# Kernel optimization log

Hardware: AMD Instinct MI355X
Metric: run time of the kernel (lower is better)

Reference implementation:

```python
import jax, jax.numpy as jnp
import numpy as np

N = 50000      # nodes
E = 800000     # edges (avg degree 16)
G = 256        # graphs in batch
DIN = 126      # input feature dim (hardcoded in module)
H = 128        # dim_h


def _lin_init(key, fan_in, shape):
    s = 1.0 / np.sqrt(fan_in)
    return jax.random.uniform(key, shape, minval=-s, maxval=s, dtype=jnp.float32)


def setup_inputs() -> dict:
    key = jax.random.key(0)
    ks = iter(jax.random.split(key, 64))
    inp = {}
    inp["x"] = jax.random.normal(next(ks), (N, DIN), dtype=jnp.float32)
    inp["edge_attr"] = jax.random.normal(next(ks), (E, 4), dtype=jnp.float32)  # unused by the conv (edge_dim=None)
    dims = [(DIN, H), (H, H), (H, H)]
    for l, (i, o) in enumerate(dims, start=1):
        for nm, bnm in [("Wk", "bk"), ("Wq", "bq"), ("Wv", "bv"), ("Ws", "bs")]:
            inp[f"{nm}{l}"] = _lin_init(next(ks), i, (i, o))
            inp[f"{bnm}{l}"] = _lin_init(next(ks), i, (o,))
    inp["W4"] = _lin_init(next(ks), H, (H, 64))
    inp["b4"] = _lin_init(next(ks), H, (64,))
    inp["W5"] = _lin_init(next(ks), 64, (64, 1))
    inp["b5"] = _lin_init(next(ks), 64, (1,))
    inp["edge_index"] = jax.random.randint(next(ks), (2, E), 0, N, dtype=jnp.int64)
    inp["batch"] = jnp.sort(jax.random.randint(next(ks), (N,), 0, G, dtype=jnp.int64))
    return inp


def _res_gated_conv(x, src, dst, Wk, bk, Wq, bq, Wv, bv, Ws, bs):
    # PyG ResGatedGraphConv: out_i = skip(x_i) + sum_j sigmoid(K_i + Q_j) * V_j
    K = x @ Wk + bk   # [N, H] keys (destination / x_i)
    Q = x @ Wq + bq   # [N, H] queries (source / x_j)
    V = x @ Wv + bv   # [N, H] values (source / x_j)
    gate = jax.nn.sigmoid(K[dst] + Q[src])           # [E, H]
    msg = gate * V[src]                              # [E, H]
    agg = jax.ops.segment_sum(msg, dst, num_segments=x.shape[0])  # scatter-add to dst
    return agg + x @ Ws + bs  # lin_skip (no bias) + conv bias


def reference(x, edge_attr,
              Wk1, bk1, Wq1, bq1, Wv1, bv1, Ws1, bs1,
              Wk2, bk2, Wq2, bq2, Wv2, bv2, Ws2, bs2,
              Wk3, bk3, Wq3, bq3, Wv3, bv3, Ws3, bs3,
              W4, b4, W5, b5, edge_index, batch):
    src, dst = edge_index[0], edge_index[1]
    h = jax.nn.relu(_res_gated_conv(x, src, dst, Wk1, bk1, Wq1, bq1, Wv1, bv1, Ws1, bs1))
    h = jax.nn.relu(_res_gated_conv(h, src, dst, Wk2, bk2, Wq2, bq2, Wv2, bv2, Ws2, bs2))
    h = _res_gated_conv(h, src, dst, Wk3, bk3, Wq3, bq3, Wv3, bv3, Ws3, bs3)
    # global_add_pool over graphs
    hg = jax.ops.segment_sum(h, batch, num_segments=G)  # [G, H]
    hg = jax.nn.relu(hg @ W4 + b4)
    return jax.nn.sigmoid(hg @ W5 + b5)  # [G, 1]
```

## Files before the change

### kernel.cpp

```cpp
#include <hip/hip_runtime.h>

#define N_NODES 50000
#define N_EDGES 800000
#define N_GRAPHS 256
#define DIN 126
#define H 128
#define MP 50048
#define NBKT 196
#define NBA 100
#define CHA 8000

typedef __attribute__((ext_vector_type(8))) _Float16 half8v;
typedef __attribute__((ext_vector_type(4))) _Float16 half4v;
typedef __attribute__((ext_vector_type(4))) float f32x4;
typedef __attribute__((ext_vector_type(2))) float f32x2;

__global__ __launch_bounds__(256) void conv_A(const float* __restrict__ X, int M, int Kd,
                                              _Float16* __restrict__ A16)
{
    const int t = blockIdx.x * 256 + threadIdx.x;
    const int row = t >> 4;
    if (row >= MP) return;
    const int k0 = (t & 15) * 8;
    half8v v8;
    #pragma unroll
    for (int j = 0; j < 8; ++j) {
        const int k = k0 + j;
        float v = 0.f;
        if (row < M && k < Kd) v = X[(size_t)row * Kd + k];
        v8[j] = (_Float16)v;
    }
    *(half8v*)&A16[(size_t)row * 128 + k0] = v8;
}

struct WPtrs { const float* w[12]; };

__global__ __launch_bounds__(256) void conv_W3(WPtrs P, _Float16* __restrict__ Wt16)
{
    const int t = blockIdx.x * 256 + threadIdx.x;
    if (t >= 3 * 512 * 128) return;
    const int layer = t >> 16;
    const int r = t & 65535;
    const int n = r >> 7, k = r & 127;
    const int mtx = n >> 7, cc = n & 127;
    const int Kd = (layer == 0) ? DIN : H;
    const float* W = P.w[layer * 4 + mtx];
    const float v = (k < Kd) ? W[(size_t)k * 128 + cc] : 0.f;
    Wt16[t] = (_Float16)v;
}

__device__ __forceinline__ void dense_out(const uint2 (&ldsO)[64][32],
                                          unsigned char* __restrict__ dst,
                                          int row0, int M, int t)
{
    #pragma unroll
    for (int i = 0; i < 4; ++i) {
        const int idx = i * 256 + t;
        const int rr = idx >> 4, c16 = idx & 15;
        const int ch = c16 ^ ((rr & 15) >> 1);
        const uint2 a = ldsO[rr][2 * ch];
        const uint2 b = ldsO[rr][2 * ch + 1];
        if (row0 + rr < M) {
            uint4 o;
            if (rr & 1) { o.x = b.x; o.y = b.y; o.z = a.x; o.w = a.y; }
            else        { o.x = a.x; o.y = a.y; o.z = b.x; o.w = b.y; }
            *(uint4*)(dst + (size_t)(row0 + rr) * 256 + c16 * 16) = o;
        }
    }
}

__device__ __forceinline__ void compute_acc(const _Float16 (&ldsA)[2][64 * 64],
                                            const _Float16* __restrict__ Wt16,
                                            int mtx, int fr, int kq, int wc,
                                            f32x4 (&acc)[4][2])
{
    #pragma unroll
    for (int step = 0; step < 4; ++step) {
        const int kg = step * 4 + kq;
        const int kh = kg >> 3, kk = kg & 7;
        half8v a[4];
        #pragma unroll
        for (int m = 0; m < 4; ++m) {
            const int ar = m * 16 + fr;
            const int slot = kk ^ (ar & 7);
            a[m] = *(const half8v*)&ldsA[kh][ar * 64 + slot * 8];
        }
        half8v w[2];
        #pragma unroll
        for (int n = 0; n < 2; ++n) {
            const size_t wo = (size_t)(mtx * 128 + wc * 32 + n * 16 + fr) * 128 + kg * 8;
            w[n] = *(const half8v*)&Wt16[wo];
        }
        #pragma unroll
        for (int m = 0; m < 4; ++m)
            #pragma unroll
            for (int n = 0; n < 2; ++n)
                acc[m][n] = __builtin_amdgcn_mfma_f32_16x16x32_f16(w[n], a[m], acc[m][n], 0, 0, 0);
    }
}

__global__ __launch_bounds__(256, 5) void gemm_mfma(
    const _Float16* __restrict__ A16, const _Float16* __restrict__ Wt16,
    const float* __restrict__ bias0, const float* __restrict__ bias1,
    const float* __restrict__ bias2, const float* __restrict__ bias3,
    _Float16* __restrict__ OEK, unsigned char* __restrict__ QV8,
    _Float16* __restrict__ OS, int M)
{
    __shared__ _Float16 ldsA[2][64 * 64];
    __shared__ uint2 ldsO[64][32];
    const int t = threadIdx.x;
    const int l = t & 63, wc = t >> 6;
    const int row0 = blockIdx.x * 64;
    const int mp = blockIdx.y;
    const int fr = l & 15;
    const int kq = l >> 4;

    #pragma unroll
    for (int i = 0; i < 4; ++i) {
        const int gi = i * 256 + t;
        const int kh = gi >> 9;
        const int r = (gi >> 3) & 63;
        const int j = gi & 7;
        const int slot = j ^ (r & 7);
        *(half8v*)&ldsA[kh][r * 64 + slot * 8] =
            *(const half8v*)&A16[(size_t)(row0 + r) * 128 + kh * 64 + j * 8];
    }
    __syncthreads();

    if (mp == 0) {
        {
            f32x4 acc[4][2] = {};
            compute_acc(ldsA, Wt16, 0, fr, kq, wc, acc);
            #pragma unroll
            for (int n = 0; n < 2; ++n) {
                const int c0 = wc * 32 + n * 16 + kq * 4;
                const float4 bv = *(const float4*)&bias0[c0];
                #pragma unroll
                for (int m = 0; m < 4; ++m) {
                    const int rl = m * 16 + fr;
                    half4v o;
                    o[0] = (_Float16)__expf(-(acc[m][n][0] + bv.x));
                    o[1] = (_Float16)__expf(-(acc[m][n][1] + bv.y));
                    o[2] = (_Float16)__expf(-(acc[m][n][2] + bv.z));
                    o[3] = (_Float16)__expf(-(acc[m][n][3] + bv.w));
                    ldsO[rl][(c0 >> 2) ^ fr] = *(uint2*)&o;
                }
            }
        }
        __syncthreads();
        dense_out(ldsO, (unsigned char*)OEK, row0, M, t);
        __syncthreads();
        {
            f32x4 acc[4][2] = {};
            compute_acc(ldsA, Wt16, 3, fr, kq, wc, acc);
            #pragma unroll
            for (int n = 0; n < 2; ++n) {
                const int c0 = wc * 32 + n * 16 + kq * 4;
                const float4 bv = *(const float4*)&bias3[c0];
                #pragma unroll
                for (int m = 0; m < 4; ++m) {
                    const int rl = m * 16 + fr;
                    half4v o;
                    o[0] = (_Float16)(acc[m][n][0] + bv.x);
                    o[1] = (_Float16)(acc[m][n][1] + bv.y);
                    o[2] = (_Float16)(acc[m][n][2] + bv.z);
                    o[3] = (_Float16)(acc[m][n][3] + bv.w);
                    ldsO[rl][(c0 >> 2) ^ fr] = *(uint2*)&o;
                }
            }
        }
        __syncthreads();
        dense_out(ldsO, (unsigned char*)OS, row0, M, t);
    } else {
        {
            f32x4 acc[4][2] = {};
            compute_acc(ldsA, Wt16, 1, fr, kq, wc, acc);
            #pragma unroll
            for (int n = 0; n < 2; ++n) {
                const int c0 = wc * 32 + n * 16 + kq * 4;
                const float4 bv = *(const float4*)&bias1[c0];
                #pragma unroll
                for (int m = 0; m < 4; ++m) {
                    const int rl = m * 16 + fr;
                    const float e0 = __expf(-(acc[m][n][0] + bv.x));
                    const float e1 = __expf(-(acc[m][n][1] + bv.y));
                    const float e2 = __expf(-(acc[m][n][2] + bv.z));
                    const float e3 = __expf(-(acc[m][n][3] + bv.w));
                    int p = 0;
                    p = __builtin_amdgcn_cvt_pk_fp8_f32(e0, e1, p, false);
                    p = __builtin_amdgcn_cvt_pk_fp8_f32(e2, e3, p, true);
                    ((unsigned*)&ldsO[rl][(c0 >> 2) ^ fr])[0] = (unsigned)p;
                }
            }
        }
        {
            f32x4 acc[4][2] = {};
            compute_acc(ldsA, Wt16, 2, fr, kq, wc, acc);
            #pragma unroll
            for (int n = 0; n < 2; ++n) {
                const int c0 = wc * 32 + n * 16 + kq * 4;
                const float4 bv = *(const float4*)&bias2[c0];
                #pragma unroll
                for (int m = 0; m < 4; ++m) {
                    const int rl = m * 16 + fr;
                    int p = 0;
                    p = __builtin_amdgcn_cvt_pk_fp8_f32(acc[m][n][0] + bv.x,
                                                        acc[m][n][1] + bv.y, p, false);
                    p = __builtin_amdgcn_cvt_pk_fp8_f32(acc[m][n][2] + bv.z,
                                                        acc[m][n][3] + bv.w, p, true);
                    ((unsigned*)&ldsO[rl][(c0 >> 2) ^ fr])[1] = (unsigned)p;
                }
            }
        }
        __syncthreads();
        dense_out(ldsO, QV8, row0, M, t);
    }
}

__global__ __launch_bounds__(256) void pA_hist(const int* __restrict__ ei,
                                               int* __restrict__ ghA)
{
    __shared__ int lh[NBKT];
    const int t = threadIdx.x, b = blockIdx.x;
    if (t < NBKT) lh[t] = 0;
    __syncthreads();
    const int e0 = b * CHA;
    for (int i = t; i < CHA; i += 256)
        atomicAdd(&lh[ei[N_EDGES + e0 + i] >> 8], 1);
    __syncthreads();
    if (t < NBKT) ghA[t * NBA + b] = lh[t];
}

__global__ __launch_bounds__(1024) void pA_scan(int* __restrict__ g)
{
    __shared__ int part[1024];
    const int t = threadIdx.x;
    const int NT = NBKT * NBA;
    const int CH = 20;
    const int base = t * CH;
    int s = 0;
    for (int i = 0; i < CH; ++i) {
        const int idx = base + i;
        if (idx < NT) s += g[idx];
    }
    part[t] = s;
    __syncthreads();
    for (int d = 1; d < 1024; d <<= 1) {
        const int v = (t >= d) ? part[t - d] : 0;
        __syncthreads();
        part[t] += v;
        __syncthreads();
    }
    int run = (t == 0) ? 0 : part[t - 1];
    for (int i = 0; i < CH; ++i) {
        const int idx = base + i;
        if (idx < NT) { const int c = g[idx]; g[idx] = run; run += c; }
    }
    if (t == 1023) g[NT] = part[1023];
}

__global__ __launch_bounds__(256) void pA_scat(const int* __restrict__ ei,
                                               const int* __restrict__ gbase,
                                               unsigned int* __restrict__ ebuf)
{
    __shared__ int cur[NBKT];
    const int t = threadIdx.x, b = blockIdx.x;
    if (t < NBKT) cur[t] = gbase[t * NBA + b];
    __syncthreads();
    const int e0 = b * CHA;
    for (int i = t; i < CHA; i += 256) {
        const unsigned d = (unsigned)ei[N_EDGES + e0 + i];
        const unsigned s = (unsigned)ei[e0 + i];
        const int pos = atomicAdd(&cur[d >> 8], 1);
        ebuf[pos] = (d << 16) | s;
    }
}

__global__ __launch_bounds__(256) void pB_build(const unsigned int* __restrict__ ebuf,
                                                const int* __restrict__ gbase,
                                                int* __restrict__ off,
                                                int* __restrict__ csr)
{
    __shared__ int lh[256], sc[256];
    const int t = threadIdx.x, b = blockIdx.x;
    const int beg = gbase[b * NBA];
    const int end = gbase[(b + 1) * NBA];
    lh[t] = 0;
    __syncthreads();
    for (int i = beg + t; i < end; i += 256)
        atomicAdd(&lh[(ebuf[i] >> 16) & 255], 1);
    __syncthreads();
    const int c = lh[t];
    sc[t] = c;
    __syncthreads();
    for (int d = 1; d < 256; d <<= 1) {
        const int v = (t >= d) ? sc[t - d] : 0;
        __syncthreads();
        sc[t] += v;
        __syncthreads();
    }
    const int excl = sc[t] - c;
    const int nd = b * 256 + t;
    if (nd <= N_NODES) off[nd] = beg + excl;
    __syncthreads();
    lh[t] = beg + excl;
    __syncthreads();
    for (int i = beg + t; i < end; i += 256) {
        const unsigned p = ebuf[i];
        const int pos = atomicAdd(&lh[(p >> 16) & 255], 1);
        csr[pos] = (int)(p & 0xFFFFu);
    }
}

template<int FUSE>
__global__ __launch_bounds__(256) void agg_csr(
    const _Float16* __restrict__ EKb, const unsigned char* __restrict__ QV8,
    const int* __restrict__ off, const int* __restrict__ csr_src,
    _Float16* __restrict__ hSkip, _Float16* __restrict__ A16, int Nn)
{
    const int node = blockIdx.x * 4 + (threadIdx.x >> 6);
    if (node >= Nn) return;
    const int lane = threadIdx.x & 63;
    const int grp = lane >> 4;
    const int sub = lane & 15;
    const int q = sub * 8;

    const half8v ek8 = *(const half8v*)(EKb + (size_t)node * H + q);
    float ek[8];
    #pragma unroll
    for (int i = 0; i < 8; ++i) ek[i] = (float)ek8[i];
    float acc[8] = {};

    const int begin = off[node], end = off[node + 1];
    for (int j0 = begin; j0 < end; j0 += 64) {
        const int nrem = end - j0;
        const int nk = nrem < 64 ? nrem : 64;
        const int sv = (lane < nk) ? csr_src[j0 + lane] : 0;
        #pragma unroll 4
        for (int k = 0; k < nk; k += 4) {
            const int myk = k + grp;
            const int s = __shfl(sv, myk < nk ? myk : 0);
            if (myk < nk) {
                const uint4 p = *(const uint4*)(QV8 + (size_t)s * 256 + sub * 16);
                const f32x2 ea = __builtin_amdgcn_cvt_pk_f32_fp8(p.x, false);
                const f32x2 eb = __builtin_amdgcn_cvt_pk_f32_fp8(p.x, true);
                const f32x2 va = __builtin_amdgcn_cvt_pk_f32_fp8(p.y, false);
                const f32x2 vb = __builtin_amdgcn_cvt_pk_f32_fp8(p.y, true);
                const f32x2 ec = __builtin_amdgcn_cvt_pk_f32_fp8(p.z, false);
                const f32x2 ed = __builtin_amdgcn_cvt_pk_f32_fp8(p.z, true);
                const f32x2 vc = __builtin_amdgcn_cvt_pk_f32_fp8(p.w, false);
                const f32x2 vd = __builtin_amdgcn_cvt_pk_f32_fp8(p.w, true);
                acc[0] = fmaf(va[0], __builtin_amdgcn_rcpf(fmaf(ek[0], ea[0], 1.f)), acc[0]);
                acc[1] = fmaf(va[1], __builtin_amdgcn_rcpf(fmaf(ek[1], ea[1], 1.f)), acc[1]);
                acc[2] = fmaf(vb[0], __builtin_amdgcn_rcpf(fmaf(ek[2], eb[0], 1.f)), acc[2]);
                acc[3] = fmaf(vb[1], __builtin_amdgcn_rcpf(fmaf(ek[3], eb[1], 1.f)), acc[3]);
                acc[4] = fmaf(vc[0], __builtin_amdgcn_rcpf(fmaf(ek[4], ec[0], 1.f)), acc[4]);
                acc[5] = fmaf(vc[1], __builtin_amdgcn_rcpf(fmaf(ek[5], ec[1], 1.f)), acc[5]);
                acc[6] = fmaf(vd[0], __builtin_amdgcn_rcpf(fmaf(ek[6], ed[0], 1.f)), acc[6]);
                acc[7] = fmaf(vd[1], __builtin_amdgcn_rcpf(fmaf(ek[7], ed[1], 1.f)), acc[7]);
            }
        }
    }
    #pragma unroll
    for (int i = 0; i < 8; ++i) {
        acc[i] += __shfl_xor(acc[i], 16);
        acc[i] += __shfl_xor(acc[i], 32);
    }
    if (grp == 0) {
        const half8v sk8 = *(const half8v*)(hSkip + (size_t)node * H + q);
        half8v hv;
        if (FUSE) {
            #pragma unroll
            for (int j = 0; j < 8; ++j)
                hv[j] = (_Float16)fmaxf((float)sk8[j] + acc[j], 0.f);
            *(half8v*)&A16[(size_t)node * 128 + q] = hv;
        } else {
            #pragma unroll
            for (int j = 0; j < 8; ++j)
                hv[j] = (_Float16)((float)sk8[j] + acc[j]);
            *(half8v*)&hSkip[(size_t)node * H + q] = hv;
        }
    }
}

__global__ __launch_bounds__(256) void gstart_kernel(const int* __restrict__ batch,
                                                     int* __restrict__ gstart, int Nn)
{
    const int n = blockIdx.x * 256 + threadIdx.x;
    if (n >= Nn) return;
    const int b = batch[n];
    const int bp = (n == 0) ? -1 : batch[n - 1];
    for (int g = bp + 1; g <= b; ++g) gstart[g] = n;
    if (n == Nn - 1)
        for (int g = b + 1; g <= N_GRAPHS; ++g) gstart[g] = Nn;
}

__global__ __launch_bounds__(128) void pool_seg(const _Float16* __restrict__ h,
                                                const int* __restrict__ gstart,
                                                float* __restrict__ hg)
{
    const int g = blockIdx.x;
    const int part = blockIdx.y;
    const int t = threadIdx.x;
    const int b0 = gstart[g], b1 = gstart[g + 1];
    float acc = 0.f;
    for (int n = b0 + part; n < b1; n += 4) acc += (float)h[(size_t)n * H + t];
    atomicAdd(&hg[(size_t)g * H + t], acc);
}

__global__ __launch_bounds__(64) void mlp_kernel(
    const float* __restrict__ hg,
    const float* __restrict__ W4, const float* __restrict__ b4,
    const float* __restrict__ W5, const float* __restrict__ b5,
    float* __restrict__ out)
{
    const int g = blockIdx.x;
    const int c = threadIdx.x;
    __shared__ float hrow[H];
    for (int k = c; k < H; k += 64) hrow[k] = hg[(size_t)g * H + k];
    __syncthreads();
    float s = b4[c];
    #pragma unroll 8
    for (int k = 0; k < H; ++k) s += hrow[k] * W4[(size_t)k * 64 + c];
    s = fmaxf(s, 0.f) * W5[c];
    #pragma unroll
    for (int off = 32; off > 0; off >>= 1) s += __shfl_down(s, off);
    if (c == 0) out[g] = 1.f / (1.f + __expf(-(s + b5[0])));
}

extern "C" void kernel_launch(void* const* d_in, const int* in_sizes, int n_in,
                              void* d_out, int out_size, void* d_ws, size_t ws_size,
                              hipStream_t stream)
{
    const float* x = (const float*)d_in[0];
    const float *Wk[3], *bk[3], *Wq[3], *bq[3], *Wv[3], *bv[3], *Wsk[3], *bs[3];
    for (int l = 0; l < 3; ++l) {
        const int base = 2 + l * 8;
        Wk[l]  = (const float*)d_in[base + 0]; bk[l] = (const float*)d_in[base + 1];
        Wq[l]  = (const float*)d_in[base + 2]; bq[l] = (const float*)d_in[base + 3];
        Wv[l]  = (const float*)d_in[base + 4]; bv[l] = (const float*)d_in[base + 5];
        Wsk[l] = (const float*)d_in[base + 6]; bs[l] = (const float*)d_in[base + 7];
    }
    const float* W4 = (const float*)d_in[26];
    const float* b4 = (const float*)d_in[27];
    const float* W5 = (const float*)d_in[28];
    const float* b5 = (const float*)d_in[29];
    const int* ei    = (const int*)d_in[30];
    const int* batch = (const int*)d_in[31];
    float* out = (float*)d_out;

    const size_t NH = (size_t)N_NODES * H;
    const size_t AH = (size_t)MP * 128;
    const size_t WH3 = (size_t)3 * 512 * 128;
    _Float16*      EKb  = (_Float16*)d_ws;
    _Float16*      hbuf = EKb + NH;
    unsigned char* QV8  = (unsigned char*)(hbuf + NH);
    _Float16*      A16  = (_Float16*)(QV8 + 2 * NH);
    _Float16*      Wt16 = A16 + AH;
    float*         hg   = (float*)(Wt16 + WH3);
    int*           off  = (int*)(hg + (size_t)N_GRAPHS * H);
    int*           csr  = off + (N_NODES + 1);
    unsigned int*  ebuf = (unsigned int*)(csr + N_EDGES);
    int*           ghA  = (int*)(ebuf + N_EDGES);
    int*           gst  = ghA + (NBKT * NBA + 1);
    const size_t need = (size_t)N_GRAPHS * H * sizeof(float)
                      + 2 * NH * sizeof(unsigned char)
                      + (2 * NH + AH + WH3) * sizeof(_Float16)
                      + (size_t)(N_NODES + 1 + 2 * N_EDGES + NBKT * NBA + 1
                                 + N_GRAPHS + 1) * sizeof(int);
    if (ws_size < need) return;

    const int ablk = (N_NODES + 3) / 4;
    const int nblk = (N_NODES + 255) / 256;
    const int cablk = (MP * 16) / 256;
    const dim3 ggrid(MP / 64, 2);
    const dim3 pgrid(N_GRAPHS, 4);

    hipMemsetAsync(hg, 0, (size_t)N_GRAPHS * H * sizeof(float), stream);

    pA_hist<<<NBA, 256, 0, stream>>>(ei, ghA);
    pA_scan<<<1, 1024, 0, stream>>>(ghA);
    pA_scat<<<NBA, 256, 0, stream>>>(ei, ghA, ebuf);
    pB_build<<<NBKT, 256, 0, stream>>>(ebuf, ghA, off, csr);
    gstart_kernel<<<nblk, 256, 0, stream>>>(batch, gst, N_NODES);
    WPtrs wp;
    for (int l = 0; l < 3; ++l) {
        wp.w[l * 4 + 0] = Wk[l];
        wp.w[l * 4 + 1] = Wq[l];
        wp.w[l * 4 + 2] = Wv[l];
        wp.w[l * 4 + 3] = Wsk[l];
    }
    conv_W3<<<768, 256, 0, stream>>>(wp, Wt16);

    conv_A<<<cablk, 256, 0, stream>>>(x, N_NODES, DIN, A16);
    gemm_mfma<<<ggrid, 256, 0, stream>>>(A16, Wt16,
        bk[0], bq[0], bv[0], bs[0], EKb, QV8, hbuf, N_NODES);
    agg_csr<1><<<ablk, 256, 0, stream>>>(EKb, QV8, off, csr, hbuf, A16, N_NODES);

    gemm_mfma<<<ggrid, 256, 0, stream>>>(A16, Wt16 + 512 * 128,
        bk[1], bq[1], bv[1], bs[1], EKb, QV8, hbuf, N_NODES);
    agg_csr<1><<<ablk, 256, 0, stream>>>(EKb, QV8, off, csr, hbuf, A16, N_NODES);

    gemm_mfma<<<ggrid, 256, 0, stream>>>(A16, Wt16 + 1024 * 128,
        bk[2], bq[2], bv[2], bs[2], EKb, QV8, hbuf, N_NODES);
    agg_csr<0><<<ablk, 256, 0, stream>>>(EKb, QV8, off, csr, hbuf, A16, N_NODES);

    pool_seg<<<pgrid, 128, 0, stream>>>(hbuf, gst, hg);
    mlp_kernel<<<N_GRAPHS, 64, 0, stream>>>(hg, W4, b4, W5, b5, out);
}
```

Measured before the change: 318.5 us.

## Use 512-thread GEMM blocks computing all four projections per row tile

The dense projection kernel moves from a 2D grid, where each 256-thread block handled two of the four weight matrices, to a 1D grid of 512-thread blocks. Each block loads its 64-row A tile into LDS once and computes K, Q/V and skip in sequence, with eight waves each owning 16 output columns. This halves redundant A-tile loads and block launches, in exchange for lower per-wave MFMA work, more barriers per block and a change in occupancy.

```diff
diff --git a/kernel.cpp b/kernel.cpp
--- a/kernel.cpp
+++ b/kernel.cpp
@@ -49,13 +49,13 @@
     Wt16[t] = (_Float16)v;
 }
 
-__device__ __forceinline__ void dense_out(const uint2 (&ldsO)[64][32],
-                                          unsigned char* __restrict__ dst,
-                                          int row0, int M, int t)
-{
-    #pragma unroll
-    for (int i = 0; i < 4; ++i) {
-        const int idx = i * 256 + t;
+__device__ __forceinline__ void dense_out512(const uint2 (&ldsO)[64][32],
+                                             unsigned char* __restrict__ dst,
+                                             int row0, int M, int t)
+{
+    #pragma unroll
+    for (int i = 0; i < 2; ++i) {
+        const int idx = i * 512 + t;
         const int rr = idx >> 4, c16 = idx & 15;
         const int ch = c16 ^ ((rr & 15) >> 1);
         const uint2 a = ldsO[rr][2 * ch];
@@ -69,10 +69,10 @@
     }
 }
 
-__device__ __forceinline__ void compute_acc(const _Float16 (&ldsA)[2][64 * 64],
-                                            const _Float16* __restrict__ Wt16,
-                                            int mtx, int fr, int kq, int wc,
-                                            f32x4 (&acc)[4][2])
+__device__ __forceinline__ void compute_acc16(const _Float16 (&ldsA)[2][64 * 64],
+                                              const _Float16* __restrict__ Wt16,
+                                              int mtx, int fr, int kq, int colbase,
+                                              f32x4 (&acc)[4])
 {
     #pragma unroll
     for (int step = 0; step < 4; ++step) {
@@ -85,21 +85,15 @@
             const int slot = kk ^ (ar & 7);
             a[m] = *(const half8v*)&ldsA[kh][ar * 64 + slot * 8];
         }
-        half8v w[2];
-        #pragma unroll
-        for (int n = 0; n < 2; ++n) {
-            const size_t wo = (size_t)(mtx * 128 + wc * 32 + n * 16 + fr) * 128 + kg * 8;
-            w[n] = *(const half8v*)&Wt16[wo];
-        }
+        const size_t wo = (size_t)(mtx * 128 + colbase + fr) * 128 + kg * 8;
+        const half8v w = *(const half8v*)&Wt16[wo];
         #pragma unroll
         for (int m = 0; m < 4; ++m)
-            #pragma unroll
-            for (int n = 0; n < 2; ++n)
-                acc[m][n] = __builtin_amdgcn_mfma_f32_16x16x32_f16(w[n], a[m], acc[m][n], 0, 0, 0);
-    }
-}
-
-__global__ __launch_bounds__(256, 5) void gemm_mfma(
+            acc[m] = __builtin_amdgcn_mfma_f32_16x16x32_f16(w, a[m], acc[m], 0, 0, 0);
+    }
+}
+
+__global__ __launch_bounds__(512) void gemm_mfma(
     const _Float16* __restrict__ A16, const _Float16* __restrict__ Wt16,
     const float* __restrict__ bias0, const float* __restrict__ bias1,
     const float* __restrict__ bias2, const float* __restrict__ bias3,
@@ -109,15 +103,15 @@
     __shared__ _Float16 ldsA[2][64 * 64];
     __shared__ uint2 ldsO[64][32];
     const int t = threadIdx.x;
-    const int l = t & 63, wc = t >> 6;
+    const int l = t & 63, w = t >> 6;
     const int row0 = blockIdx.x * 64;
-    const int mp = blockIdx.y;
     const int fr = l & 15;
     const int kq = l >> 4;
-
-    #pragma unroll
-    for (int i = 0; i < 4; ++i) {
-        const int gi = i * 256 + t;
+    const int colbase = w * 16;
+
+    #pragma unroll
+    for (int i = 0; i < 2; ++i) {
+        const int gi = i * 512 + t;
         const int kh = gi >> 9;
         const int r = (gi >> 3) & 63;
         const int j = gi & 7;
@@ -127,94 +121,81 @@
     }
     __syncthreads();
 
-    if (mp == 0) {
-        {
-            f32x4 acc[4][2] = {};
-            compute_acc(ldsA, Wt16, 0, fr, kq, wc, acc);
-            #pragma unroll
-            for (int n = 0; n < 2; ++n) {
-                const int c0 = wc * 32 + n * 16 + kq * 4;
-                const float4 bv = *(const float4*)&bias0[c0];
-                #pragma unroll
-                for (int m = 0; m < 4; ++m) {
-                    const int rl = m * 16 + fr;
-                    half4v o;
-                    o[0] = (_Float16)__expf(-(acc[m][n][0] + bv.x));
-                    o[1] = (_Float16)__expf(-(acc[m][n][1] + bv.y));
-                    o[2] = (_Float16)__expf(-(acc[m][n][2] + bv.z));
-                    o[3] = (_Float16)__expf(-(acc[m][n][3] + bv.w));
-                    ldsO[rl][(c0 >> 2) ^ fr] = *(uint2*)&o;
-                }
-            }
-        }
-        __syncthreads();
-        dense_out(ldsO, (unsigned char*)OEK, row0, M, t);
-        __syncthreads();
-        {
-            f32x4 acc[4][2] = {};
-            compute_acc(ldsA, Wt16, 3, fr, kq, wc, acc);
-            #pragma unroll
-            for (int n = 0; n < 2; ++n) {
-                const int c0 = wc * 32 + n * 16 + kq * 4;
-                const float4 bv = *(const float4*)&bias3[c0];
-                #pragma unroll
-                for (int m = 0; m < 4; ++m) {
-                    const int rl = m * 16 + fr;
-                    half4v o;
-                    o[0] = (_Float16)(acc[m][n][0] + bv.x);
-                    o[1] = (_Float16)(acc[m][n][1] + bv.y);
-                    o[2] = (_Float16)(acc[m][n][2] + bv.z);
-                    o[3] = (_Float16)(acc[m][n][3] + bv.w);
-                    ldsO[rl][(c0 >> 2) ^ fr] = *(uint2*)&o;
-                }
-            }
-        }
-        __syncthreads();
-        dense_out(ldsO, (unsigned char*)OS, row0, M, t);
-    } else {
-        {
-            f32x4 acc[4][2] = {};
-            compute_acc(ldsA, Wt16, 1, fr, kq, wc, acc);
-            #pragma unroll
-            for (int n = 0; n < 2; ++n) {
-                const int c0 = wc * 32 + n * 16 + kq * 4;
-                const float4 bv = *(const float4*)&bias1[c0];
-                #pragma unroll
-                for (int m = 0; m < 4; ++m) {
-                    const int rl = m * 16 + fr;
-                    const float e0 = __expf(-(acc[m][n][0] + bv.x));
-                    const float e1 = __expf(-(acc[m][n][1] + bv.y));
-                    const float e2 = __expf(-(acc[m][n][2] + bv.z));
-                    const float e3 = __expf(-(acc[m][n][3] + bv.w));
-                    int p = 0;
-                    p = __builtin_amdgcn_cvt_pk_fp8_f32(e0, e1, p, false);
-                    p = __builtin_amdgcn_cvt_pk_fp8_f32(e2, e3, p, true);
-                    ((unsigned*)&ldsO[rl][(c0 >> 2) ^ fr])[0] = (unsigned)p;
-                }
-            }
-        }
-        {
-            f32x4 acc[4][2] = {};
-            compute_acc(ldsA, Wt16, 2, fr, kq, wc, acc);
-            #pragma unroll
-            for (int n = 0; n < 2; ++n) {
-                const int c0 = wc * 32 + n * 16 + kq * 4;
-                const float4 bv = *(const float4*)&bias2[c0];
-                #pragma unroll
-                for (int m = 0; m < 4; ++m) {
-                    const int rl = m * 16 + fr;
-                    int p = 0;
-                    p = __builtin_amdgcn_cvt_pk_fp8_f32(acc[m][n][0] + bv.x,
-                                                        acc[m][n][1] + bv.y, p, false);
-                    p = __builtin_amdgcn_cvt_pk_fp8_f32(acc[m][n][2] + bv.z,
-                                                        acc[m][n][3] + bv.w, p, true);
-                    ((unsigned*)&ldsO[rl][(c0 >> 2) ^ fr])[1] = (unsigned)p;
-                }
-            }
-        }
-        __syncthreads();
-        dense_out(ldsO, QV8, row0, M, t);
-    }
+    const int c0 = colbase + kq * 4;
+    const int qd = (c0 >> 2) ^ fr;
+
+    {
+        f32x4 acc[4] = {};
+        compute_acc16(ldsA, Wt16, 0, fr, kq, colbase, acc);
+        const float4 bv = *(const float4*)&bias0[c0];
+        #pragma unroll
+        for (int m = 0; m < 4; ++m) {
+            const int rl = m * 16 + fr;
+            half4v o;
+            o[0] = (_Float16)__expf(-(acc[m][0] + bv.x));
+            o[1] = (_Float16)__expf(-(acc[m][1] + bv.y));
+            o[2] = (_Float16)__expf(-(acc[m][2] + bv.z));
+            o[3] = (_Float16)__expf(-(acc[m][3] + bv.w));
+            ldsO[rl][qd] = *(uint2*)&o;
+        }
+    }
+    __syncthreads();
+    dense_out512(ldsO, (unsigned char*)OEK, row0, M, t);
+    __syncthreads();
+
+    {
+        f32x4 acc[4] = {};
+        compute_acc16(ldsA, Wt16, 1, fr, kq, colbase, acc);
+        const float4 bv = *(const float4*)&bias1[c0];
+        #pragma unroll
+        for (int m = 0; m < 4; ++m) {
+            const int rl = m * 16 + fr;
+            const float e0 = __expf(-(acc[m][0] + bv.x));
+            const float e1 = __expf(-(acc[m][1] + bv.y));
+            const float e2 = __expf(-(acc[m][2] + bv.z));
+            const float e3 = __expf(-(acc[m][3] + bv.w));
+            int p = 0;
+            p = __builtin_amdgcn_cvt_pk_fp8_f32(e0, e1, p, false);
+            p = __builtin_amdgcn_cvt_pk_fp8_f32(e2, e3, p, true);
+            ((unsigned*)&ldsO[rl][qd])[0] = (unsigned)p;
+        }
+    }
+    {
+        f32x4 acc[4] = {};
+        compute_acc16(ldsA, Wt16, 2, fr, kq, colbase, acc);
+        const float4 bv = *(const float4*)&bias2[c0];
+        #pragma unroll
+        for (int m = 0; m < 4; ++m) {
+            const int rl = m * 16 + fr;
+            int p = 0;
+            p = __builtin_amdgcn_cvt_pk_fp8_f32(acc[m][0] + bv.x,
+                                                acc[m][1] + bv.y, p, false);
+            p = __builtin_amdgcn_cvt_pk_fp8_f32(acc[m][2] + bv.z,
+                                                acc[m][3] + bv.w, p, true);
+            ((unsigned*)&ldsO[rl][qd])[1] = (unsigned)p;
+        }
+    }
+    __syncthreads();
+    dense_out512(ldsO, QV8, row0, M, t);
+    __syncthreads();
+
+    {
+        f32x4 acc[4] = {};
+        compute_acc16(ldsA, Wt16, 3, fr, kq, colbase, acc);
+        const float4 bv = *(const float4*)&bias3[c0];
+        #pragma unroll
+        for (int m = 0; m < 4; ++m) {
+            const int rl = m * 16 + fr;
+            half4v o;
+            o[0] = (_Float16)(acc[m][0] + bv.x);
+            o[1] = (_Float16)(acc[m][1] + bv.y);
+            o[2] = (_Float16)(acc[m][2] + bv.z);
+            o[3] = (_Float16)(acc[m][3] + bv.w);
+            ldsO[rl][qd] = *(uint2*)&o;
+        }
+    }
+    __syncthreads();
+    dense_out512(ldsO, (unsigned char*)OS, row0, M, t);
 }
 
 __global__ __launch_bounds__(256) void pA_hist(const int* __restrict__ ei,
@@ -473,7 +454,7 @@
     const int ablk = (N_NODES + 3) / 4;
     const int nblk = (N_NODES + 255) / 256;
     const int cablk = (MP * 16) / 256;
-    const dim3 ggrid(MP / 64, 2);
+    const int ggrid = MP / 64;
     const dim3 pgrid(N_GRAPHS, 4);
 
     hipMemsetAsync(hg, 0, (size_t)N_GRAPHS * H * sizeof(float), stream);
@@ -493,15 +474,15 @@
     conv_W3<<<768, 256, 0, stream>>>(wp, Wt16);
 
     conv_A<<<cablk, 256, 0, stream>>>(x, N_NODES, DIN, A16);
-    gemm_mfma<<<ggrid, 256, 0, stream>>>(A16, Wt16,
+    gemm_mfma<<<ggrid, 512, 0, stream>>>(A16, Wt16,
         bk[0], bq[0], bv[0], bs[0], EKb, QV8, hbuf, N_NODES);
     agg_csr<1><<<ablk, 256, 0, stream>>>(EKb, QV8, off, csr, hbuf, A16, N_NODES);
 
-    gemm_mfma<<<ggrid, 256, 0, stream>>>(A16, Wt16 + 512 * 128,
+    gemm_mfma<<<ggrid, 512, 0, stream>>>(A16, Wt16 + 512 * 128,
         bk[1], bq[1], bv[1], bs[1], EKb, QV8, hbuf, N_NODES);
     agg_csr<1><<<ablk, 256, 0, stream>>>(EKb, QV8, off, csr, hbuf, A16, N_NODES);
 
-    gemm_mfma<<<ggrid, 256, 0, stream>>>(A16, Wt16 + 1024 * 128,
+    gemm_mfma<<<ggrid, 512, 0, stream>>>(A16, Wt16 + 1024 * 128,
         bk[2], bq[2], bv[2], bs[2], EKb, QV8, hbuf, N_NODES);
     agg_csr<0><<<ablk, 256, 0, stream>>>(EKb, QV8, off, csr, hbuf, A16, N_NODES);
 
```

Measured after the change: 296.9 us. 6.8% less time.
